# Optimization experiments

Measured on AMD Instinct MI355X. Metric: run time of the kernel, lower is better.

## Reference

```python
import jax, jax.numpy as jnp
import numpy as np

IN_C = 64
OUT_C = 128
HEADS = 8
DIM = 9 * IN_C  # 576


def unfold3x3_s2(fea):
    # torch.nn.functional.unfold(fea, (3,3), padding=1, stride=2)
    # returns [N, C*9, L] with channel-major (c, kh, kw) ordering.
    N, C, H, W = fea.shape
    Ho, Wo = H // 2, W // 2
    p = jnp.pad(fea, ((0, 0), (0, 0), (1, 1), (1, 1)))
    patches = jnp.stack(
        [p[:, :, ki:ki + 2 * Ho:2, kj:kj + 2 * Wo:2] for ki in range(3) for kj in range(3)],
        axis=2,
    )  # [N, C, 9, Ho, Wo]
    return patches.reshape(N, C * 9, Ho * Wo)


def mhsa(x, w_qkv, b_qkv, w_out, b_out):
    # standard ViT attention: x [B, L, D]
    B, L, D = x.shape
    dh = D // HEADS
    qkv = x @ w_qkv + b_qkv  # [B, L, 3D]
    q, k, v = jnp.split(qkv, 3, axis=-1)
    def heads(t):
        return t.reshape(B, L, HEADS, dh).transpose(0, 2, 1, 3)  # [B, h, L, dh]
    q, k, v = heads(q), heads(k), heads(v)
    scale = dh ** -0.5
    scores = jnp.einsum('bhqd,bhkd->bhqk', q, k) * scale
    attn = jax.nn.softmax(scores, axis=-1)
    o = jnp.einsum('bhqk,bhkd->bhqd', attn, v)  # [B, h, L, dh]
    o = o.transpose(0, 2, 1, 3).reshape(B, L, D)
    return o @ w_out + b_out


def setup_inputs() -> dict:
    key = jax.random.key(0)
    ks = jax.random.split(key, 6)
    s = DIM ** -0.5
    return {
        'fea': jax.random.normal(ks[0], (1, IN_C, 128, 128), dtype=jnp.float32),
        'w_qkv': jax.random.normal(ks[1], (DIM, 3 * DIM), dtype=jnp.float32) * s,
        'b_qkv': jnp.zeros((3 * DIM,), dtype=jnp.float32),
        'w_out': jax.random.normal(ks[2], (DIM, DIM), dtype=jnp.float32) * s,
        'b_out': jnp.zeros((DIM,), dtype=jnp.float32),
        'conv_w': jax.random.normal(ks[3], (OUT_C, IN_C, 3, 3), dtype=jnp.float32) * s,
    }


def reference(fea, w_qkv, b_qkv, w_out, b_out, conv_w):
    N, C, H, W = fea.shape
    Ho, Wo = H // 2, W // 2
    x = unfold3x3_s2(fea).transpose(0, 2, 1)          # [N, L, 9C]
    x = mhsa(x, w_qkv, b_qkv, w_out, b_out) + x       # residual
    # matmul with reshaped conv weights: [N, L, 9C] @ [9C, out_c]
    y = x @ conv_w.reshape(OUT_C, -1).T               # [N, L, out_c]
    y = y.transpose(0, 2, 1).reshape(N, OUT_C, Ho, Wo)  # fold with (1,1) kernel
    return jax.nn.silu(y)
```

## Files before the change

kernel.cpp:

```cpp
#include <hip/hip_runtime.h>
#include <hip/hip_bf16.h>
#include <math.h>

#define L_TOK 4096
#define D_DIM 576
#define NHEADS 8
#define DHEAD 72
#define DPAD 96
#define HSZ ((size_t)NHEADS * L_TOK * DPAD)
#define KSPLIT 4
#define LOG2E 1.4426950408889634f

typedef __attribute__((ext_vector_type(8))) short short8;
typedef __attribute__((ext_vector_type(4))) short short4v;
typedef __attribute__((ext_vector_type(4))) float float4v;

union F4S8 {
  float4 f4;
  short8 s8;
  __hip_bfloat16 h[8];
};

__device__ inline void tc_body(const float* __restrict__ src,
                               __hip_bfloat16* __restrict__ dst, int R, int C,
                               int bi, int bj, int t, __hip_bfloat16* Ts) {
  const int col = t & 63, row4 = t >> 6;
#pragma unroll
  for (int u = 0; u < 16; u++) {
    int r = u * 4 + row4;
    Ts[r * 68 + col] = __float2bfloat16(src[(size_t)(bj * 64 + r) * C + bi * 64 + col]);
  }
  __syncthreads();
#pragma unroll
  for (int u = 0; u < 16; u++) {
    int c = u * 4 + row4;
    dst[(size_t)(bi * 64 + c) * R + bj * 64 + col] = Ts[col * 68 + c];
  }
}

__global__ __launch_bounds__(256) void prep_all(const float* __restrict__ fea,
                                                const float* __restrict__ w_qkv,
                                                const float* __restrict__ w_out,
                                                const float* __restrict__ conv_w,
                                                __hip_bfloat16* __restrict__ xb,
                                                __hip_bfloat16* __restrict__ WqkvT,
                                                __hip_bfloat16* __restrict__ WoT,
                                                __hip_bfloat16* __restrict__ CwB) {
  __shared__ float Shm[3120];
  const int b = blockIdx.x;
  const int t = threadIdx.x;
  if (b < 512) {
    float* Lf = Shm;
    const int ho = b & 63;
    const int c0 = (b >> 6) * 8;
    for (int e = t; e < 3072; e += 256) {
      int c = e / 384;
      int rr = (e / 128) % 3;
      int w = e & 127;
      int h = 2 * ho + rr - 1;
      float v = 0.f;
      if ((unsigned)h < 128u) v = fea[(size_t)(c0 + c) * 16384 + h * 128 + w];
      Lf[(c * 3 + rr) * 130 + w + 1] = v;
    }
    if (t < 24) { Lf[t * 130] = 0.f; Lf[t * 130 + 129] = 0.f; }
    __syncthreads();
    for (int e = t; e < 576; e += 256) {
      int wo = e / 9, ch = e - wo * 9;
      F4S8 u;
#pragma unroll
      for (int j = 0; j < 8; j++) {
        int dd = ch * 8 + j;
        int c = dd / 9, k = dd - c * 9;
        int ki = k / 3, kj = k - ki * 3;
        u.h[j] = __float2bfloat16(Lf[(c * 3 + ki) * 130 + 2 * wo + kj]);
      }
      *(float4*)(xb + (size_t)(ho * 64 + wo) * D_DIM + c0 * 9 + ch * 8) = u.f4;
    }
  } else if (b < 755) {
    int bb = b - 512;
    tc_body(w_qkv, WqkvT, D_DIM, 1728, bb % 27, bb / 27, t, (__hip_bfloat16*)Shm);
  } else if (b < 836) {
    int bb = b - 755;
    tc_body(w_out, WoT, D_DIM, D_DIM, bb % 9, bb / 9, t, (__hip_bfloat16*)Shm);
  } else {
    int i = (b - 836) * 256 + t;
    CwB[i] = __float2bfloat16(conv_w[i]);
  }
}

template <int EPI, int NMI>
__global__ __launch_bounds__(256) void gemm_mfma(const __hip_bfloat16* __restrict__ A,
                                                 const __hip_bfloat16* __restrict__ Bt,
                                                 const float* __restrict__ bias,
                                                 const __hip_bfloat16* __restrict__ resid,
                                                 __hip_bfloat16* __restrict__ outB,
                                                 __hip_bfloat16* __restrict__ outB2) {
  constexpr int K = D_DIM;
  constexpr int BM = NMI * 32;
  __shared__ __align__(16) __hip_bfloat16 As[BM * 72];
  __shared__ __align__(16) __hip_bfloat16 Bs[64 * 72];
  const int t = threadIdx.x;
  const int wave = t >> 6, lane = t & 63, quad = lane >> 4, l16 = lane & 15;
  const int wm = (wave & 2) * (NMI * 8);
  const int wn = (wave & 1) * 32;
  const int m0 = blockIdx.x * BM, n0 = blockIdx.y * 64;

  float4v acc[NMI][2];
#pragma unroll
  for (int i = 0; i < NMI; i++)
#pragma unroll
    for (int j = 0; j < 2; j++) acc[i][j] = (float4v){0.f, 0.f, 0.f, 0.f};

  const int arow = t >> 3, ach = t & 7;
  for (int k0 = 0; k0 < K; k0 += 64) {
    __syncthreads();
#pragma unroll
    for (int u = 0; u < NMI; u++) {
      int row = u * 32 + arow;
      *(float4*)(&As[row * 72 + ach * 8]) =
          *(const float4*)(A + (size_t)(m0 + row) * K + k0 + ach * 8);
    }
#pragma unroll
    for (int u = 0; u < 2; u++) {
      int row = u * 32 + arow;
      *(float4*)(&Bs[row * 72 + ach * 8]) =
          *(const float4*)(Bt + (size_t)(n0 + row) * K + k0 + ach * 8);
    }
    __syncthreads();
    short8 af[NMI][2], bfr[2][2];
#pragma unroll
    for (int i = 0; i < NMI; i++)
#pragma unroll
      for (int s = 0; s < 2; s++)
        af[i][s] = *(const short8*)(&As[(wm + i * 16 + l16) * 72 + s * 32 + quad * 8]);
#pragma unroll
    for (int j = 0; j < 2; j++)
#pragma unroll
      for (int s = 0; s < 2; s++)
        bfr[j][s] = *(const short8*)(&Bs[(wn + j * 16 + l16) * 72 + s * 32 + quad * 8]);
#pragma unroll
    for (int i = 0; i < NMI; i++)
#pragma unroll
      for (int j = 0; j < 2; j++) {
        acc[i][j] = __builtin_amdgcn_mfma_f32_16x16x32_bf16(af[i][0], bfr[j][0], acc[i][j], 0, 0, 0);
        acc[i][j] = __builtin_amdgcn_mfma_f32_16x16x32_bf16(af[i][1], bfr[j][1], acc[i][j], 0, 0, 0);
      }
  }

  if (EPI == 0) {
    const int part = n0 / D_DIM;
    if (part < 2) {
      __hip_bfloat16* dst = outB + (size_t)part * HSZ;
#pragma unroll
      for (int j = 0; j < 2; j++) {
        int ng = n0 + wn + j * 16 + l16;
        float bv = bias[ng];
        int rem = ng - part * D_DIM;
        int h = rem / DHEAD;
        int d = rem - h * DHEAD;
#pragma unroll
        for (int i = 0; i < NMI; i++) {
          int mb = m0 + wm + i * 16 + quad * 4;
#pragma unroll
          for (int r = 0; r < 4; r++)
            dst[((size_t)h * L_TOK + mb + r) * DPAD + d] = __float2bfloat16(acc[i][j][r] + bv);
        }
      }
    } else {
      __hip_bfloat16* Ls = As;
      __syncthreads();
      const int n0rel = n0 - 2 * D_DIM;
#pragma unroll
      for (int j = 0; j < 2; j++) {
        int nloc = wn + j * 16 + l16;
        float bv = bias[n0 + nloc];
#pragma unroll
        for (int i = 0; i < NMI; i++) {
          int mloc = wm + i * 16 + quad * 4;
#pragma unroll
          for (int r = 0; r < 4; r++)
            Ls[nloc * 136 + mloc + r] = __float2bfloat16(acc[i][j][r] + bv);
        }
      }
      __syncthreads();
      for (int e = t; e < 1024; e += 256) {
        int row = e >> 4, ch = e & 15;
        int ng = n0rel + row;
        int hh = ng / DHEAD, dd = ng - hh * DHEAD;
        *(float4*)(outB2 + ((size_t)hh * DPAD + dd) * L_TOK + m0 + ch * 8) =
            *(const float4*)(&Ls[row * 136 + ch * 8]);
      }
    }
  } else {
#pragma unroll
    for (int j = 0; j < 2; j++) {
      int ng = n0 + wn + j * 16 + l16;
      float bv = bias[ng];
#pragma unroll
      for (int i = 0; i < NMI; i++) {
        int mb = m0 + wm + i * 16 + quad * 4;
#pragma unroll
        for (int r = 0; r < 4; r++) {
          size_t idx = (size_t)(mb + r) * D_DIM + ng;
          float v = acc[i][j][r] + bv + __bfloat162float(resid[idx]);
          outB[idx] = __float2bfloat16(v);
        }
      }
    }
  }
}

__global__ __launch_bounds__(256) void final_small(const __hip_bfloat16* __restrict__ A,
                                                   const __hip_bfloat16* __restrict__ Bt,
                                                   float* __restrict__ out) {
  __shared__ __align__(16) __hip_bfloat16 As[32 * 72];
  __shared__ __align__(16) __hip_bfloat16 Bs[32 * 72];
  const int t = threadIdx.x;
  const int wave = t >> 6, lane = t & 63, quad = lane >> 4, l16 = lane & 15;
  const int wm = (wave & 2) * 8;
  const int wn = (wave & 1) * 16;
  const int m0 = blockIdx.x * 32, n0 = blockIdx.y * 32;

  float4v acc = (float4v){0.f, 0.f, 0.f, 0.f};

  const int arow = t >> 3, ach = t & 7;
  for (int k0 = 0; k0 < D_DIM; k0 += 64) {
    __syncthreads();
    *(float4*)(&As[arow * 72 + ach * 8]) =
        *(const float4*)(A + (size_t)(m0 + arow) * D_DIM + k0 + ach * 8);
    *(float4*)(&Bs[arow * 72 + ach * 8]) =
        *(const float4*)(Bt + (size_t)(n0 + arow) * D_DIM + k0 + ach * 8);
    __syncthreads();
    short8 af[2], bfr[2];
#pragma unroll
    for (int s = 0; s < 2; s++) {
      af[s] = *(const short8*)(&As[(wm + l16) * 72 + s * 32 + quad * 8]);
      bfr[s] = *(const short8*)(&Bs[(wn + l16) * 72 + s * 32 + quad * 8]);
    }
    acc = __builtin_amdgcn_mfma_f32_16x16x32_bf16(af[0], bfr[0], acc, 0, 0, 0);
    acc = __builtin_amdgcn_mfma_f32_16x16x32_bf16(af[1], bfr[1], acc, 0, 0, 0);
  }
  const int oc = n0 + wn + l16;
  const int mb = m0 + wm + quad * 4;
#pragma unroll
  for (int r = 0; r < 4; r++) {
    float v = acc[r];
    float sg = 1.f / (1.f + __expf(-v));
    out[(size_t)oc * L_TOK + mb + r] = v * sg;
  }
}

#define KS_STRIDE 104
#define VT_STRIDE 72
#define PS_STRIDE 40
#define KBUF (64 * KS_STRIDE)
#define VBUF (80 * VT_STRIDE)
#define MSHIFT 8.0f

__global__ __launch_bounds__(256, 2) void attn_mfma(const __hip_bfloat16* __restrict__ Qb,
                                                    const __hip_bfloat16* __restrict__ Kb,
                                                    const __hip_bfloat16* __restrict__ VbT,
                                                    __hip_bfloat16* __restrict__ Opart,
                                                    float* __restrict__ Ml) {
  __shared__ __align__(16) __hip_bfloat16 Ks[2 * KBUF];
  __shared__ __align__(16) __hip_bfloat16 Vt[2 * VBUF];
  __shared__ __align__(16) __hip_bfloat16 Ps[4 * 64 * PS_STRIDE];

  const int bid = blockIdx.x;
  const int h = bid & 7;
  const int rest = bid >> 3;
  const int ksp = rest & 3;
  const int qblk = rest >> 2;
  const int t = threadIdx.x;
  const int wave = t >> 6;
  const int lane = t & 63;
  const int quad = lane >> 4;
  const int l16 = lane & 15;

  const __hip_bfloat16* Qh = Qb + (size_t)h * L_TOK * DPAD;
  const __hip_bfloat16* Kh = Kb + (size_t)h * L_TOK * DPAD;
  const __hip_bfloat16* VhT = VbT + (size_t)h * DPAD * L_TOK;

  const int qbase = qblk * 256 + wave * 64;
  short8 qf[4][3];
#pragma unroll
  for (int mi = 0; mi < 4; mi++) {
#pragma unroll
    for (int s = 0; s < 3; s++) {
      if (s == 2 && quad >= 1) {
        qf[mi][s] = (short8){0, 0, 0, 0, 0, 0, 0, 0};
      } else {
        qf[mi][s] = *(const short8*)(Qh + (size_t)(qbase + mi * 16 + l16) * DPAD + s * 32 + quad * 8);
      }
    }
  }

  const float4 zero4 = {0.f, 0.f, 0.f, 0.f};
  if (t < 192) {
    int row = t / 3, ch = 9 + t % 3;
    *(float4*)(&Ks[row * KS_STRIDE + ch * 8]) = zero4;
    *(float4*)(&Ks[KBUF + row * KS_STRIDE + ch * 8]) = zero4;
  } else {
    int e = t - 192;
    int d = 72 + (e >> 3), ch = e & 7;
    *(float4*)(&Vt[d * VT_STRIDE + ch * 8]) = zero4;
    *(float4*)(&Vt[VBUF + d * VT_STRIDE + ch * 8]) = zero4;
  }

  float4v Of[4][5];
#pragma unroll
  for (int mi = 0; mi < 4; mi++)
#pragma unroll
    for (int nt = 0; nt < 5; nt++) Of[mi][nt] = (float4v){0.f, 0.f, 0.f, 0.f};
  float lrow[4] = {0.f, 0.f, 0.f, 0.f};
  const float scale2 = 0.11785113019775792f * LOG2E;

  __hip_bfloat16* myPs = Ps + wave * 64 * PS_STRIDE;
  const int kstart = ksp * 1024;

  auto stage = [&](int kbase, __hip_bfloat16* Kw, __hip_bfloat16* Vw) {
    for (int e = t; e < 576; e += 256) {
      int row = e / 9, ch = e - row * 9;
      *(float4*)(&Kw[row * KS_STRIDE + ch * 8]) =
          *(const float4*)(Kh + (size_t)(kbase + row) * DPAD + ch * 8);
    }
    for (int e = t; e < 576; e += 256) {
      int d = e >> 3, ch = e & 7;
      *(float4*)(&Vw[d * VT_STRIDE + ch * 8]) =
          *(const float4*)(VhT + (size_t)d * L_TOK + kbase + ch * 8);
    }
  };

  stage(kstart, Ks, Vt);
  __syncthreads();

  for (int kt = 0; kt < 16; kt++) {
    const int p = kt & 1;
    if (kt + 1 < 16)
      stage(kstart + (kt + 1) * 64, Ks + (1 - p) * KBUF, Vt + (1 - p) * VBUF);

    const __hip_bfloat16* Ksb = Ks + p * KBUF;
    const __hip_bfloat16* Vtb = Vt + p * VBUF;

    float4v S[4][4];
#pragma unroll
    for (int ks = 0; ks < 4; ks++) {
      float4v a0 = (float4v){0.f, 0.f, 0.f, 0.f};
      float4v a1 = a0, a2 = a0, a3 = a0;
#pragma unroll
      for (int s = 0; s < 3; s++) {
        short8 kf = *(const short8*)(&Ksb[(ks * 16 + l16) * KS_STRIDE + s * 32 + quad * 8]);
        a0 = __builtin_amdgcn_mfma_f32_16x16x32_bf16(kf, qf[0][s], a0, 0, 0, 0);
        a1 = __builtin_amdgcn_mfma_f32_16x16x32_bf16(kf, qf[1][s], a1, 0, 0, 0);
        a2 = __builtin_amdgcn_mfma_f32_16x16x32_bf16(kf, qf[2][s], a2, 0, 0, 0);
        a3 = __builtin_amdgcn_mfma_f32_16x16x32_bf16(kf, qf[3][s], a3, 0, 0, 0);
      }
#pragma unroll
      for (int r = 0; r < 4; r++) {
        S[0][ks][r] = a0[r]; S[1][ks][r] = a1[r];
        S[2][ks][r] = a2[r]; S[3][ks][r] = a3[r];
      }
    }

#pragma unroll
    for (int kstep = 0; kstep < 2; kstep++) {
#pragma unroll
      for (int mi = 0; mi < 4; mi++) {
#pragma unroll
        for (int k2 = 0; k2 < 2; k2++) {
          int ks = kstep * 2 + k2;
          union { short4v v; __hip_bfloat16 hh[4]; } pk;
#pragma unroll
          for (int r = 0; r < 4; r++) {
            float pr = exp2f(fmaf(S[mi][ks][r], scale2, -MSHIFT));
            lrow[mi] += pr;
            pk.hh[r] = __float2bfloat16(pr);
          }
          *(short4v*)(&myPs[(mi * 16 + l16) * PS_STRIDE + k2 * 16 + quad * 4]) = pk.v;
        }
      }
      short8 pa[4];
#pragma unroll
      for (int mi = 0; mi < 4; mi++)
        pa[mi] = *(const short8*)(&myPs[(mi * 16 + l16) * PS_STRIDE + quad * 8]);
#pragma unroll
      for (int nt = 0; nt < 5; nt++) {
        short8 vb = *(const short8*)(&Vtb[(nt * 16 + l16) * VT_STRIDE + kstep * 32 + quad * 8]);
        Of[0][nt] = __builtin_amdgcn_mfma_f32_16x16x32_bf16(pa[0], vb, Of[0][nt], 0, 0, 0);
        Of[1][nt] = __builtin_amdgcn_mfma_f32_16x16x32_bf16(pa[1], vb, Of[1][nt], 0, 0, 0);
        Of[2][nt] = __builtin_amdgcn_mfma_f32_16x16x32_bf16(pa[2], vb, Of[2][nt], 0, 0, 0);
        Of[3][nt] = __builtin_amdgcn_mfma_f32_16x16x32_bf16(pa[3], vb, Of[3][nt], 0, 0, 0);
      }
    }

    __syncthreads();
  }

#pragma unroll
  for (int mi = 0; mi < 4; mi++) {
    lrow[mi] += __shfl_xor(lrow[mi], 16);
    lrow[mi] += __shfl_xor(lrow[mi], 32);
  }

  const size_t pb = ((size_t)ksp * NHEADS + h) * L_TOK;
#pragma unroll
  for (int mi = 0; mi < 4; mi++) {
#pragma unroll
    for (int nt = 0; nt < 5; nt++) {
      int d = nt * 16 + l16;
      if (d < DHEAD) {
#pragma unroll
        for (int r = 0; r < 4; r++) {
          int q = qbase + mi * 16 + quad * 4 + r;
          Opart[(pb + q) * 72 + d] = __float2bfloat16(Of[mi][nt][r]);
        }
      }
    }
  }
  if (quad == 0) {
#pragma unroll
    for (int mi = 0; mi < 4; mi++) {
      int q = qbase + mi * 16 + l16;
      Ml[pb + q] = lrow[mi];
    }
  }
}

__global__ __launch_bounds__(256) void attn_merge(const __hip_bfloat16* __restrict__ Opart,
                                                  const float* __restrict__ Ml,
                                                  __hip_bfloat16* __restrict__ ob) {
  int idx = blockIdx.x * 256 + threadIdx.x;
  int h = idx / (L_TOK * 9);
  int rem = idx - h * (L_TOK * 9);
  int q = rem / 9;
  int ch = rem - q * 9;
  float denom = 0.f;
  float acc[8] = {0, 0, 0, 0, 0, 0, 0, 0};
#pragma unroll
  for (int s = 0; s < KSPLIT; s++) {
    size_t b = ((size_t)s * NHEADS + h) * L_TOK + q;
    denom += Ml[b];
    short8 o = *(const short8*)(Opart + b * 72 + ch * 8);
#pragma unroll
    for (int j = 0; j < 8; j++) {
      union { short ss; __hip_bfloat16 bb; } u;
      u.ss = o[j];
      acc[j] += __bfloat162float(u.bb);
    }
  }
  float inv = 1.f / denom;
  __hip_bfloat16* dst = ob + (size_t)q * D_DIM + h * DHEAD + ch * 8;
#pragma unroll
  for (int j = 0; j < 8; j++) dst[j] = __float2bfloat16(acc[j] * inv);
}

extern "C" void kernel_launch(void* const* d_in, const int* in_sizes, int n_in,
                              void* d_out, int out_size, void* d_ws, size_t ws_size,
                              hipStream_t stream) {
  const float* fea    = (const float*)d_in[0];
  const float* w_qkv  = (const float*)d_in[1];
  const float* b_qkv  = (const float*)d_in[2];
  const float* w_out  = (const float*)d_in[3];
  const float* b_out  = (const float*)d_in[4];
  const float* conv_w = (const float*)d_in[5];
  float* out = (float*)d_out;

  __hip_bfloat16* xb    = (__hip_bfloat16*)d_ws;
  __hip_bfloat16* WqkvT = xb + (size_t)L_TOK * D_DIM;
  __hip_bfloat16* WoT   = WqkvT + (size_t)1728 * D_DIM;
  __hip_bfloat16* CwB   = WoT + (size_t)D_DIM * D_DIM;
  __hip_bfloat16* QKb   = CwB + (size_t)128 * D_DIM;
  __hip_bfloat16* VbT   = QKb + 2 * HSZ;
  __hip_bfloat16* Opart = VbT + HSZ;
  float* Ml = (float*)(Opart + (size_t)KSPLIT * NHEADS * L_TOK * 72);
  __hip_bfloat16* ob = QKb;
  __hip_bfloat16* xr = Opart;

  prep_all<<<1124, 256, 0, stream>>>(fea, w_qkv, w_out, conv_w, xb, WqkvT, WoT, CwB);
  gemm_mfma<0, 4><<<dim3(32, 27), 256, 0, stream>>>(xb, WqkvT, b_qkv, nullptr, QKb, VbT);
  attn_mfma<<<512, 256, 0, stream>>>(QKb, QKb + HSZ, VbT, Opart, Ml);
  attn_merge<<<1152, 256, 0, stream>>>(Opart, Ml, ob);
  gemm_mfma<1, 2><<<dim3(64, 9), 256, 0, stream>>>(ob, WoT, b_out, xb, xr, nullptr);
  final_small<<<dim3(128, 4), 256, 0, stream>>>(xr, CwB, out);
}
```

Baseline: 188.1 us.

## Fold softmax scale and shift into Q/K padding and compute row sums via MFMA

The softmax scale (times log2e) is folded into Q when the QKV projection writes it. A constant -8 shift goes into a padded Q column that multiplies a 1.0 in the padded K column, so the score MFMA yields the shifted, scaled logit directly. A ones row in the padded V columns makes the PV MFMA produce the row sum of P in an extra output column, which replaces the per-element lrow accumulation and the shuffle reduction. This trims VALU work from the exp loop, at the cost of rounding the scale into bf16 Q and summing the bf16-rounded P values instead of fp32 ones.

```diff
diff --git a/kernel.cpp b/kernel.cpp
--- a/kernel.cpp
+++ b/kernel.cpp
@@ -10,6 +10,7 @@
 #define HSZ ((size_t)NHEADS * L_TOK * DPAD)
 #define KSPLIT 4
 #define LOG2E 1.4426950408889634f
+#define SCALE2 (0.11785113019775792f * 1.4426950408889634f)
 
 typedef __attribute__((ext_vector_type(8))) short short8;
 typedef __attribute__((ext_vector_type(4))) short short4v;
@@ -151,6 +152,7 @@
     const int part = n0 / D_DIM;
     if (part < 2) {
       __hip_bfloat16* dst = outB + (size_t)part * HSZ;
+      const float sc = (part == 0) ? SCALE2 : 1.f;
 #pragma unroll
       for (int j = 0; j < 2; j++) {
         int ng = n0 + wn + j * 16 + l16;
@@ -163,7 +165,8 @@
           int mb = m0 + wm + i * 16 + quad * 4;
 #pragma unroll
           for (int r = 0; r < 4; r++)
-            dst[((size_t)h * L_TOK + mb + r) * DPAD + d] = __float2bfloat16(acc[i][j][r] + bv);
+            dst[((size_t)h * L_TOK + mb + r) * DPAD + d] =
+                __float2bfloat16((acc[i][j][r] + bv) * sc);
         }
       }
     } else {
@@ -255,7 +258,6 @@
 #define PS_STRIDE 40
 #define KBUF (64 * KS_STRIDE)
 #define VBUF (80 * VT_STRIDE)
-#define MSHIFT 8.0f
 
 __global__ __launch_bounds__(256, 2) void attn_mfma(const __hip_bfloat16* __restrict__ Qb,
                                                     const __hip_bfloat16* __restrict__ Kb,
@@ -289,6 +291,7 @@
     for (int s = 0; s < 3; s++) {
       if (s == 2 && quad >= 1) {
         qf[mi][s] = (short8){0, 0, 0, 0, 0, 0, 0, 0};
+        if (quad == 1) qf[mi][s][0] = (short)0xC100;
       } else {
         qf[mi][s] = *(const short8*)(Qh + (size_t)(qbase + mi * 16 + l16) * DPAD + s * 32 + quad * 8);
       }
@@ -296,15 +299,20 @@
   }
 
   const float4 zero4 = {0.f, 0.f, 0.f, 0.f};
+  union { float4 f4; unsigned u[4]; } kpad, vones;
+  kpad.u[0] = 0x00003F80u; kpad.u[1] = 0u; kpad.u[2] = 0u; kpad.u[3] = 0u;
+  vones.u[0] = vones.u[1] = vones.u[2] = vones.u[3] = 0x3F803F80u;
   if (t < 192) {
     int row = t / 3, ch = 9 + t % 3;
-    *(float4*)(&Ks[row * KS_STRIDE + ch * 8]) = zero4;
-    *(float4*)(&Ks[KBUF + row * KS_STRIDE + ch * 8]) = zero4;
+    float4 kv = (ch == 9) ? kpad.f4 : zero4;
+    *(float4*)(&Ks[row * KS_STRIDE + ch * 8]) = kv;
+    *(float4*)(&Ks[KBUF + row * KS_STRIDE + ch * 8]) = kv;
   } else {
     int e = t - 192;
     int d = 72 + (e >> 3), ch = e & 7;
-    *(float4*)(&Vt[d * VT_STRIDE + ch * 8]) = zero4;
-    *(float4*)(&Vt[VBUF + d * VT_STRIDE + ch * 8]) = zero4;
+    float4 vv = (d == 72) ? vones.f4 : zero4;
+    *(float4*)(&Vt[d * VT_STRIDE + ch * 8]) = vv;
+    *(float4*)(&Vt[VBUF + d * VT_STRIDE + ch * 8]) = vv;
   }
 
   float4v Of[4][5];
@@ -312,8 +320,6 @@
   for (int mi = 0; mi < 4; mi++)
 #pragma unroll
     for (int nt = 0; nt < 5; nt++) Of[mi][nt] = (float4v){0.f, 0.f, 0.f, 0.f};
-  float lrow[4] = {0.f, 0.f, 0.f, 0.f};
-  const float scale2 = 0.11785113019775792f * LOG2E;
 
   __hip_bfloat16* myPs = Ps + wave * 64 * PS_STRIDE;
   const int kstart = ksp * 1024;
@@ -372,8 +378,7 @@
           union { short4v v; __hip_bfloat16 hh[4]; } pk;
 #pragma unroll
           for (int r = 0; r < 4; r++) {
-            float pr = exp2f(fmaf(S[mi][ks][r], scale2, -MSHIFT));
-            lrow[mi] += pr;
+            float pr = exp2f(S[mi][ks][r]);
             pk.hh[r] = __float2bfloat16(pr);
           }
           *(short4v*)(&myPs[(mi * 16 + l16) * PS_STRIDE + k2 * 16 + quad * 4]) = pk.v;
@@ -396,12 +401,6 @@
     __syncthreads();
   }
 
-#pragma unroll
-  for (int mi = 0; mi < 4; mi++) {
-    lrow[mi] += __shfl_xor(lrow[mi], 16);
-    lrow[mi] += __shfl_xor(lrow[mi], 32);
-  }
-
   const size_t pb = ((size_t)ksp * NHEADS + h) * L_TOK;
 #pragma unroll
   for (int mi = 0; mi < 4; mi++) {
@@ -417,11 +416,12 @@
       }
     }
   }
-  if (quad == 0) {
+  if (l16 == 8) {
 #pragma unroll
     for (int mi = 0; mi < 4; mi++) {
-      int q = qbase + mi * 16 + l16;
-      Ml[pb + q] = lrow[mi];
+#pragma unroll
+      for (int r = 0; r < 4; r++)
+        Ml[pb + qbase + mi * 16 + quad * 4 + r] = Of[mi][4][r];
     }
   }
 }
```

New measurement: 181.5 us. -3.5%, faster.
